# Optimization experiments

Hardware: AMD Instinct MI355X
Metric: run time of the kernel (lower is better)

## Reference

```python
import jax, jax.numpy as jnp
import numpy as np

N_QUBITS = 8

def _ry(theta):
    # PennyLane RY = exp(-i theta Y/2) = [[c,-s],[s,c]]
    c = jnp.cos(theta / 2).astype(jnp.complex64)
    s = jnp.sin(theta / 2).astype(jnp.complex64)
    return jnp.stack([jnp.stack([c, -s], -1), jnp.stack([s, c], -1)], -2)

def _rz(theta):
    # PennyLane RZ = diag(e^{-i theta/2}, e^{i theta/2})
    ph = jnp.exp(-0.5j * theta.astype(jnp.complex64))
    z = jnp.zeros_like(ph)
    return jnp.stack([jnp.stack([ph, z], -1), jnp.stack([z, jnp.conj(ph)], -1)], -2)

def _apply_1q(state, U, wire):
    # state: (B, 2,...,2); U: (2,2) or (B,2,2)
    state = jnp.moveaxis(state, wire + 1, -1)
    if U.ndim == 3:
        state = jnp.einsum('bij,b...j->b...i', U, state)
    else:
        state = jnp.einsum('ij,b...j->b...i', U, state)
    return jnp.moveaxis(state, -1, wire + 1)

def _apply_cnot(state, c, t):
    state = jnp.moveaxis(state, (c + 1, t + 1), (-2, -1))
    state = jnp.concatenate([state[..., 0:1, :], state[..., 1:2, ::-1]], axis=-2)
    return jnp.moveaxis(state, (-2, -1), (c + 1, t + 1))

def _circuit(angles, qw):
    # angles: (B, 2*n_qubits), qw: (3, n_qubits, 3)
    B = angles.shape[0]
    state = jnp.zeros((B,) + (2,) * N_QUBITS, jnp.complex64)
    state = state.at[(slice(None),) + (0,) * N_QUBITS].set(1.0)
    for i in range(N_QUBITS):
        state = _apply_1q(state, _ry(angles[:, i]), i)
        state = _apply_1q(state, _rz(angles[:, i + N_QUBITS]), i)
    for layer in range(3):
        for i in range(N_QUBITS):
            phi, theta, omega = qw[layer, i]
            U = _rz(omega) @ _ry(theta) @ _rz(phi)  # Rot(phi,theta,omega)
            state = _apply_1q(state, U, i)
        for i in range(N_QUBITS - 1):
            state = _apply_cnot(state, i, i + 1)
        state = _apply_cnot(state, N_QUBITS - 1, 0)
    probs = jnp.abs(state) ** 2  # (B, 2,...,2) real
    expz = []
    for i in range(N_QUBITS):
        p = probs.sum(axis=tuple(a for a in range(1, N_QUBITS + 1) if a != i + 1))
        expz.append(p[:, 0] - p[:, 1])  # <Z_i> = p(0) - p(1)
    return jnp.stack(expz, -1)


def setup_inputs() -> dict:
    key = jax.random.key(0)
    ks = jax.random.split(key, 10)
    B = 16384
    return {
        'x': jax.random.normal(ks[0], (B, 80), jnp.float32),
        'W1': jax.random.normal(ks[1], (64, 80), jnp.float32) * 0.1,
        'b1': jax.random.normal(ks[2], (64,), jnp.float32) * 0.1,
        'W2': jax.random.normal(ks[3], (32, 64), jnp.float32) * 0.1,
        'b2': jax.random.normal(ks[4], (32,), jnp.float32) * 0.1,
        'W3': jax.random.normal(ks[5], (16, 32), jnp.float32) * 0.1,
        'b3': jax.random.normal(ks[6], (16,), jnp.float32) * 0.1,
        'qw': jax.random.normal(ks[7], (3, 8, 3), jnp.float32),
        'Wp': jax.random.normal(ks[8], (128, 8), jnp.float32) * 0.1,
        'bp': jax.random.normal(ks[9], (128,), jnp.float32) * 0.1,
    }


def reference(x, W1, b1, W2, b2, W3, b3, qw, Wp, bp):
    h = jnp.tanh(x @ W1.T + b1)
    h = jnp.tanh(h @ W2.T + b2)
    angles = h @ W3.T + b3          # (B, 16)
    z = _circuit(angles, qw)        # (B, 8) PauliZ expectations
    return z @ Wp.T + bp            # (B, 128)
```

## Files before the change

### kernel.cpp

```cpp
#include <hip/hip_runtime.h>

typedef float v2f __attribute__((ext_vector_type(2)));

#define WPB 4
#define NE  4

__device__ __forceinline__ float xorf(float v, int sb) {
  return __int_as_float(__float_as_int(v) ^ sb);
}

__device__ __forceinline__ void pkfma_ip(v2f a, v2f b, v2f& acc) {
  asm("v_pk_fma_f32 %0, %1, %2, %0" : "+v"(acc) : "v"(a), "v"(b));
}
__device__ __forceinline__ v2f pkmul_bl(v2f c, v2f v) {
  v2f r; asm("v_pk_mul_f32 %0, %1, %2 op_sel:[0,0] op_sel_hi:[0,1]"
             : "=v"(r) : "v"(c), "v"(v)); return r;
}
__device__ __forceinline__ void pkfma_bl(v2f c, v2f v, v2f& acc) {
  asm("v_pk_fma_f32 %0, %1, %2, %0 op_sel:[0,0,0] op_sel_hi:[0,1,1]"
      : "+v"(acc) : "v"(c), "v"(v));
}
__device__ __forceinline__ void pkfma_bl_n(v2f c, v2f v, v2f& acc) {
  asm("v_pk_fma_f32 %0, %1, %2, %0 op_sel:[0,0,0] op_sel_hi:[0,1,1] neg_lo:[1,0,0] neg_hi:[1,0,0]"
      : "+v"(acc) : "v"(c), "v"(v));
}
__device__ __forceinline__ void pkfma_bh_i(v2f c, v2f v, v2f& acc) {
  asm("v_pk_fma_f32 %0, %1, %2, %0 op_sel:[1,1,0] op_sel_hi:[1,0,1] neg_lo:[1,0,0]"
      : "+v"(acc) : "v"(c), "v"(v));
}
__device__ __forceinline__ void pkfma_bh_mi(v2f c, v2f v, v2f& acc) {
  asm("v_pk_fma_f32 %0, %1, %2, %0 op_sel:[1,1,0] op_sel_hi:[1,0,1] neg_hi:[1,0,0]"
      : "+v"(acc) : "v"(c), "v"(v));
}
__device__ __forceinline__ v2f cmul(v2f a, v2f b) {
  v2f r = pkmul_bl(a, b);
  pkfma_bh_i(a, b, r);
  return r;
}

template<int M>
__device__ __forceinline__ float xch(float v, int a32) {
  if constexpr (M == 32)
    return __int_as_float(__builtin_amdgcn_ds_bpermute(a32, __float_as_int(v)));
  else if constexpr (M == 16 || M == 4)
    return __int_as_float(__builtin_amdgcn_ds_swizzle(__float_as_int(v), (M << 10) | 0x1f));
  else if constexpr (M == 8) {
    int i = __float_as_int(v);
    return __int_as_float(__builtin_amdgcn_update_dpp(i, i, 0x128, 0xF, 0xF, false));
  } else if constexpr (M == 2) {
    int i = __float_as_int(v);
    return __int_as_float(__builtin_amdgcn_update_dpp(i, i, 0x4E, 0xF, 0xF, false));
  } else {
    int i = __float_as_int(v);
    return __int_as_float(__builtin_amdgcn_update_dpp(i, i, 0xB1, 0xF, 0xF, false));
  }
}
template<int M>
__device__ __forceinline__ v2f xch2(v2f v, int a32) {
  v2f r; r.x = xch<M>(v.x, a32); r.y = xch<M>(v.y, a32); return r;
}
__device__ __forceinline__ v2f bperm2(int addr, v2f v) {
  v2f r;
  r.x = __int_as_float(__builtin_amdgcn_ds_bpermute(addr, __float_as_int(v.x)));
  r.y = __int_as_float(__builtin_amdgcn_ds_bpermute(addr, __float_as_int(v.y)));
  return r;
}

__device__ __forceinline__ void gpair(v2f& a, v2f& b, v2f P1, v2f P2) {
  v2f na = pkmul_bl(P1, a);
  pkfma_bh_i(P1, a, na);
  pkfma_bl(P2, b, na);
  pkfma_bh_i(P2, b, na);
  v2f nb = pkmul_bl(P1, b);
  pkfma_bh_mi(P1, b, nb);
  pkfma_bl_n(P2, a, nb);
  pkfma_bh_i(P2, a, nb);
  a = na; b = nb;
}
__device__ __forceinline__ v2f glane(v2f a, v2f p, v2f P1, v2f P2) {
  v2f t = pkmul_bl(P1, a);
  pkfma_bh_i(P1, a, t);
  pkfma_bl(P2, p, t);
  pkfma_bh_i(P2, p, t);
  return t;
}

template<int W>
__device__ __forceinline__ void gate_all(v2f* S, v2f P1, v2f P2,
                                         const int* sb, int a32) {
  if constexpr (W == 0) {
    #pragma unroll
    for (int e = 0; e < NE; ++e) {
      gpair(S[4*e+0], S[4*e+2], P1, P2); gpair(S[4*e+1], S[4*e+3], P1, P2);
    }
  } else if constexpr (W == 1) {
    #pragma unroll
    for (int e = 0; e < NE; ++e) {
      gpair(S[4*e+0], S[4*e+1], P1, P2); gpair(S[4*e+2], S[4*e+3], P1, P2);
    }
  } else {
    constexpr int M = 1 << (7 - W);
    const int s = sb[W - 2];
    v2f P1s = P1; P1s.y = xorf(P1.y, s);
    v2f P2s = P2; P2s.x = xorf(P2.x, s);
    #pragma unroll
    for (int e = 0; e < NE; ++e) {
      v2f p0 = xch2<M>(S[4*e+0], a32), p1 = xch2<M>(S[4*e+1], a32),
          p2 = xch2<M>(S[4*e+2], a32), p3 = xch2<M>(S[4*e+3], a32);
      S[4*e+0] = glane(S[4*e+0], p0, P1s, P2s);
      S[4*e+1] = glane(S[4*e+1], p1, P1s, P2s);
      S[4*e+2] = glane(S[4*e+2], p2, P1s, P2s);
      S[4*e+3] = glane(S[4*e+3], p3, P1s, P2s);
    }
  }
}

__device__ __forceinline__ void build_state(v2f* S, const float4* csW, int lane) {
  v2f g[6];
  #pragma unroll
  for (int w = 2; w < 8; ++w) {
    float4 c = csW[w];
    v2f P1 = (v2f){c.x, c.y};
    v2f nc2 = (v2f){-c.z, c.w};
    bool shi = ((lane >> (7 - w)) & 1) != 0;
    g[w - 2] = shi ? nc2 : P1;
  }
  v2f c23 = cmul(g[0], g[1]);
  v2f c45 = cmul(g[2], g[3]);
  v2f c67 = cmul(g[4], g[5]);
  v2f common = cmul(c23, cmul(c45, c67));
  float4 c0 = csW[0], c1 = csW[1];
  v2f P10 = (v2f){c0.x, c0.y}, m0 = (v2f){-c0.z, c0.w};
  v2f P11 = (v2f){c1.x, c1.y}, m1 = (v2f){-c1.z, c1.w};
  S[0] = cmul(cmul(P10, P11), common);
  S[1] = cmul(cmul(P10, m1 ), common);
  S[2] = cmul(cmul(m0 , P11), common);
  S[3] = cmul(cmul(m0 , m1 ), common);
}

__device__ __forceinline__ void cnot_ring(v2f* S, int addrA, int addrB, int lane) {
  { v2f t = S[2]; S[2] = S[3]; S[3] = t; }
  S[0] = bperm2(addrA, S[0]); S[2] = bperm2(addrA, S[2]);
  S[1] = bperm2(addrB, S[1]); S[3] = bperm2(addrB, S[3]);
  bool c0 = (lane & 1) != 0;
  v2f t0 = S[0], t1 = S[1];
  S[0] = c0 ? S[2] : S[0]; S[2] = c0 ? t0 : S[2];
  S[1] = c0 ? S[3] : S[1]; S[3] = c0 ? t1 : S[3];
}

__device__ __forceinline__ void readout(const v2f* S, int lane, const int* sb,
                                        int a32, float* z) {
  float p0 = S[0].x*S[0].x + S[0].y*S[0].y;
  float p1 = S[1].x*S[1].x + S[1].y*S[1].y;
  float p2 = S[2].x*S[2].x + S[2].y*S[2].y;
  float p3 = S[3].x*S[3].x + S[3].y*S[3].y;
  float E = (p0 + p3) - (p1 + p2);
  float F = (p0 + p2) - (p1 + p3);
  float Fv = xorf(F, (__popc(lane) & 1) << 31);
  float Sm = E, d1, d2, d3, d4, d5, d6;
  { float p = xch<32>(Sm, a32); d1 = xorf(Sm - p, sb[0]); Sm += p; }
  { float p = xch<16>(Sm, a32); Sm += p;
    float q = xch<16>(d1, a32); d2 = xorf(d1 - q, sb[1]); d1 += q; }
  { float p = xch<8>(Sm, a32); Sm += p;
    float q = xch<8>(d1, a32); d1 += q;
    float r = xch<8>(d2, a32); d3 = xorf(d2 - r, sb[2]); d2 += r; }
  { float p = xch<4>(Sm, a32); Sm += p;
    float q = xch<4>(d1, a32); d1 += q;
    float r = xch<4>(d2, a32); d2 += r;
    float t = xch<4>(d3, a32); d4 = xorf(d3 - t, sb[3]); d3 += t; }
  { float p = xch<2>(Sm, a32); Sm += p;
    float q = xch<2>(d1, a32); d1 += q;
    float r = xch<2>(d2, a32); d2 += r;
    float t = xch<2>(d3, a32); d3 += t;
    float w = xch<2>(d4, a32); d5 = xorf(d4 - w, sb[4]); d4 += w; }
  { float p = xch<1>(Sm, a32); Sm += p;
    float q = xch<1>(d1, a32); d1 += q;
    float r = xch<1>(d2, a32); d2 += r;
    float t = xch<1>(d3, a32); d3 += t;
    float w = xch<1>(d4, a32); d4 += w;
    float v = xch<1>(d5, a32); d6 = xorf(d5 - v, sb[5]); d5 += v; }
  Fv += xch<32>(Fv, a32); Fv += xch<16>(Fv, a32); Fv += xch<8>(Fv, a32);
  Fv += xch<4>(Fv, a32);  Fv += xch<2>(Fv, a32);  Fv += xch<1>(Fv, a32);
  z[0] = Fv; z[1] = Sm; z[2] = d1; z[3] = d2;
  z[4] = d3; z[5] = d4; z[6] = d5; z[7] = d6;
}

__device__ __forceinline__ float fast_tanh(float x) {
  float e = __expf(2.f * x);
  return 1.f - 2.f * __builtin_amdgcn_rcpf(e + 1.f);
}
__device__ __forceinline__ v2f vlo(float4 v) { return (v2f){v.x, v.y}; }
__device__ __forceinline__ v2f vhi(float4 v) { return (v2f){v.z, v.w}; }

__global__ void prep_rot_kernel(const float* __restrict__ qw, float* __restrict__ U) {
  int t = threadIdx.x;
  if (t < 24) {
    float phi = qw[t*3+0], theta = qw[t*3+1], omega = qw[t*3+2];
    float st, ct; sincosf(0.5f*theta, &st, &ct);
    float sa, ca; sincosf(0.5f*(phi+omega), &sa, &ca);
    float sd, cd; sincosf(0.5f*(phi-omega), &sd, &cd);
    float4 o; o.x = ct*ca; o.y = -ct*sa; o.z = -st*cd; o.w = -st*sd;
    ((float4*)U)[t] = o;
  }
}

__global__ __launch_bounds__(64*WPB) void qblock_kernel(
    const float* __restrict__ x,  const float* __restrict__ W1, const float* __restrict__ b1,
    const float* __restrict__ W2, const float* __restrict__ b2,
    const float* __restrict__ W3, const float* __restrict__ b3,
    const float* __restrict__ Urot, const float* __restrict__ Wp, const float* __restrict__ bp,
    float* __restrict__ out, int B4)
{
  __shared__ float  h1s[WPB][NE][64];
  __shared__ float  h2s[WPB][NE][32];
  __shared__ v2f    cs [WPB][NE][16];
  __shared__ float4 csW[WPB][NE][8];

  const int lane = threadIdx.x & 63;
  const int wv   = threadIdx.x >> 6;
  int bw = blockIdx.x * WPB + wv;
  if (bw >= B4) bw = B4 - 1;
  bw = __builtin_amdgcn_readfirstlane(bw);
  const int e0 = NE * bw;
  const v2f* Ug2 = (const v2f*)Urot;

  {
    const float4* wr = (const float4*)(W1 + lane * 80);
    float bv = b1[lane];
    v2f a0[NE], a1[NE];
    #pragma unroll
    for (int e = 0; e < NE; ++e) { a0[e] = (v2f){bv, 0.f}; a1[e] = (v2f){0.f, 0.f}; }
    #pragma unroll
    for (int k = 0; k < 20; ++k) {
      float4 wk = wr[k];
      #pragma unroll
      for (int e = 0; e < NE; ++e) {
        float4 xk = ((const float4*)(x + (size_t)(e0 + e) * 80))[k];
        pkfma_ip(vlo(xk), vlo(wk), a0[e]);
        pkfma_ip(vhi(xk), vhi(wk), a1[e]);
      }
    }
    #pragma unroll
    for (int e = 0; e < NE; ++e)
      h1s[wv][e][lane] = fast_tanh((a0[e].x + a0[e].y) + (a1[e].x + a1[e].y));
  }
  __threadfence_block();

  {
    const int ep = lane >> 5, row = lane & 31;
    const float4* wr = (const float4*)(W2 + row * 64);
    const float4* hvA = (const float4*)(&h1s[wv][2*ep+0][0]);
    const float4* hvB = (const float4*)(&h1s[wv][2*ep+1][0]);
    v2f aA0 = (v2f){b2[row], 0.f}, aA1 = (v2f){0.f, 0.f};
    v2f aB0 = aA0, aB1 = aA1;
    #pragma unroll
    for (int k = 0; k < 16; ++k) {
      float4 wk = wr[k], hA = hvA[k], hB = hvB[k];
      pkfma_ip(vlo(hA), vlo(wk), aA0); pkfma_ip(vhi(hA), vhi(wk), aA1);
      pkfma_ip(vlo(hB), vlo(wk), aB0); pkfma_ip(vhi(hB), vhi(wk), aB1);
    }
    h2s[wv][2*ep+0][row] = fast_tanh((aA0.x + aA0.y) + (aA1.x + aA1.y));
    h2s[wv][2*ep+1][row] = fast_tanh((aB0.x + aB0.y) + (aB1.x + aB1.y));
  }
  __threadfence_block();

  {
    const int e = lane >> 4, row = lane & 15;
    const float4* hv = (const float4*)(&h2s[wv][e][0]);
    const float4* wr = (const float4*)(W3 + row * 32);
    v2f ac0 = (v2f){b3[row], 0.f}, ac1 = (v2f){0.f, 0.f};
    #pragma unroll
    for (int k = 0; k < 8; ++k) {
      float4 hk = hv[k], wk = wr[k];
      pkfma_ip(vlo(hk), vlo(wk), ac0);
      pkfma_ip(vhi(hk), vhi(wk), ac1);
    }
    float sh, ch; __sincosf(0.5f * ((ac0.x + ac0.y) + (ac1.x + ac1.y)), &sh, &ch);
    cs[wv][e][row] = (v2f){ch, sh};
  }
  __threadfence_block();

  if (lane < 32) {
    const int e = lane >> 3, k = lane & 7;
    v2f yy = cs[wv][e][k], zz = cs[wv][e][k + 8];
    v2f u1 = (v2f){  yy.x * zz.x, -yy.x * zz.y };
    v2f u2 = (v2f){ -yy.y * zz.x,  yy.y * zz.y };
    v2f cu1 = (v2f){ u1.x, -u1.y };
    v2f cu2 = (v2f){ u2.x, -u2.y };
    v2f r1 = Ug2[2 * k], r2 = Ug2[2 * k + 1];
    v2f P1c = cmul(r1, u1);
    pkfma_bl_n(r2, cu2, P1c);
    pkfma_bh_mi(r2, cu2, P1c);
    v2f P2c = cmul(r1, u2);
    pkfma_bl(r2, cu1, P2c);
    pkfma_bh_i(r2, cu1, P2c);
    csW[wv][e][k] = make_float4(P1c.x, P1c.y, P2c.x, P2c.y);
  }
  __threadfence_block();

  const int a32 = (lane ^ 32) << 2;
  const int sb[6] = { (lane&32)<<26, (lane&16)<<27, (lane&8)<<28,
                      (lane&4)<<29, (lane&2)<<30, (lane&1)<<31 };
  const int addrA = ((lane ^ (lane >> 1)) & 63) << 2;
  const int addrB = addrA ^ 128;

  v2f S[4 * NE];
  #pragma unroll
  for (int e = 0; e < NE; ++e) build_state(&S[4*e], &csW[wv][e][0], lane);
  #pragma unroll
  for (int e = 0; e < NE; ++e) cnot_ring(&S[4*e], addrA, addrB, lane);

  #define LGB(l, i) { v2f P1 = Ug2[((l)*8+(i))*2], P2 = Ug2[((l)*8+(i))*2+1]; \
    gate_all<i>(S, P1, P2, sb, a32); }
  LGB(1,0) LGB(1,1) LGB(1,2) LGB(1,3) LGB(1,4) LGB(1,5) LGB(1,6) LGB(1,7)
  #pragma unroll
  for (int e = 0; e < NE; ++e) cnot_ring(&S[4*e], addrA, addrB, lane);
  LGB(2,0) LGB(2,1) LGB(2,2) LGB(2,3) LGB(2,4) LGB(2,5) LGB(2,6) LGB(2,7)
  #undef LGB

  const int r0 = 2 * lane;
  const float4* wp = (const float4*)(Wp + r0 * 8);
  float4 w0v = wp[0], w1v = wp[1], w2v = wp[2], w3v = wp[3];
  float2 bpv = ((const float2*)bp)[lane];
  #pragma unroll
  for (int e = 0; e < NE; ++e) {
    float z[8];
    readout(&S[4*e], lane, sb, a32, z);
    float o0 = bpv.x + z[0]*w0v.x + z[1]*w0v.y + z[2]*w0v.z + z[3]*w0v.w
                     + z[4]*w1v.x + z[5]*w1v.y + z[6]*w1v.z + z[7]*w1v.w;
    float o1 = bpv.y + z[0]*w2v.x + z[1]*w2v.y + z[2]*w2v.z + z[3]*w2v.w
                     + z[4]*w3v.x + z[5]*w3v.y + z[6]*w3v.z + z[7]*w3v.w;
    ((float2*)(out + (size_t)(e0 + e) * 128))[lane] = make_float2(o0, o1);
  }
}

extern "C" void kernel_launch(void* const* d_in, const int* in_sizes, int n_in,
                              void* d_out, int out_size, void* d_ws, size_t ws_size,
                              hipStream_t stream) {
  const float* x  = (const float*)d_in[0];
  const float* W1 = (const float*)d_in[1];
  const float* b1 = (const float*)d_in[2];
  const float* W2 = (const float*)d_in[3];
  const float* b2 = (const float*)d_in[4];
  const float* W3 = (const float*)d_in[5];
  const float* b3 = (const float*)d_in[6];
  const float* qw = (const float*)d_in[7];
  const float* Wp = (const float*)d_in[8];
  const float* bp = (const float*)d_in[9];
  float* out = (float*)d_out;
  float* Urot = (float*)d_ws;

  const int B = in_sizes[0] / 80;
  const int B4 = B / NE;
  prep_rot_kernel<<<1, 64, 0, stream>>>(qw, Urot);
  const int grid = (B4 + WPB - 1) / WPB;
  qblock_kernel<<<grid, 64 * WPB, 0, stream>>>(x, W1, b1, W2, b2, W3, b3,
                                               Urot, Wp, bp, out, B4);
}
```

Baseline: 42.20 us.

## Process eight batch elements per wave and pair readout reductions

Doubles the number of batch elements each wavefront simulates from four to eight. The MLP stages are reshaped to cover the extra elements, and the readout reduces two states at once so each cross-lane exchange carries packed pairs. The aim is to amortise weight loads, fixed per-wave costs and shuffle latency over more elements. In exchange it raises register pressure from a doubled state array, which may lower occupancy, and halves the grid size.

New measurement: 41.87 us. About the same (-0.8%).

```diff
diff --git a/kernel.cpp b/kernel.cpp
--- a/kernel.cpp
+++ b/kernel.cpp
@@ -3,10 +3,13 @@
 typedef float v2f __attribute__((ext_vector_type(2)));
 
 #define WPB 4
-#define NE  4
+#define NE  8
 
 __device__ __forceinline__ float xorf(float v, int sb) {
   return __int_as_float(__float_as_int(v) ^ sb);
+}
+__device__ __forceinline__ v2f xor2(v2f v, int sb) {
+  return (v2f){xorf(v.x, sb), xorf(v.y, sb)};
 }
 
 __device__ __forceinline__ void pkfma_ip(v2f a, v2f b, v2f& acc) {
@@ -148,39 +151,39 @@
   S[1] = c0 ? S[3] : S[1]; S[3] = c0 ? t1 : S[3];
 }
 
-__device__ __forceinline__ void readout(const v2f* S, int lane, const int* sb,
-                                        int a32, float* z) {
-  float p0 = S[0].x*S[0].x + S[0].y*S[0].y;
-  float p1 = S[1].x*S[1].x + S[1].y*S[1].y;
-  float p2 = S[2].x*S[2].x + S[2].y*S[2].y;
-  float p3 = S[3].x*S[3].x + S[3].y*S[3].y;
-  float E = (p0 + p3) - (p1 + p2);
-  float F = (p0 + p2) - (p1 + p3);
-  float Fv = xorf(F, (__popc(lane) & 1) << 31);
-  float Sm = E, d1, d2, d3, d4, d5, d6;
-  { float p = xch<32>(Sm, a32); d1 = xorf(Sm - p, sb[0]); Sm += p; }
-  { float p = xch<16>(Sm, a32); Sm += p;
-    float q = xch<16>(d1, a32); d2 = xorf(d1 - q, sb[1]); d1 += q; }
-  { float p = xch<8>(Sm, a32); Sm += p;
-    float q = xch<8>(d1, a32); d1 += q;
-    float r = xch<8>(d2, a32); d3 = xorf(d2 - r, sb[2]); d2 += r; }
-  { float p = xch<4>(Sm, a32); Sm += p;
-    float q = xch<4>(d1, a32); d1 += q;
-    float r = xch<4>(d2, a32); d2 += r;
-    float t = xch<4>(d3, a32); d4 = xorf(d3 - t, sb[3]); d3 += t; }
-  { float p = xch<2>(Sm, a32); Sm += p;
-    float q = xch<2>(d1, a32); d1 += q;
-    float r = xch<2>(d2, a32); d2 += r;
-    float t = xch<2>(d3, a32); d3 += t;
-    float w = xch<2>(d4, a32); d5 = xorf(d4 - w, sb[4]); d4 += w; }
-  { float p = xch<1>(Sm, a32); Sm += p;
-    float q = xch<1>(d1, a32); d1 += q;
-    float r = xch<1>(d2, a32); d2 += r;
-    float t = xch<1>(d3, a32); d3 += t;
-    float w = xch<1>(d4, a32); d4 += w;
-    float v = xch<1>(d5, a32); d6 = xorf(d5 - v, sb[5]); d5 += v; }
-  Fv += xch<32>(Fv, a32); Fv += xch<16>(Fv, a32); Fv += xch<8>(Fv, a32);
-  Fv += xch<4>(Fv, a32);  Fv += xch<2>(Fv, a32);  Fv += xch<1>(Fv, a32);
+__device__ __forceinline__ void readout2(const v2f* SA, const v2f* SB,
+                                         int lane, const int* sb, int a32, v2f* z) {
+  v2f p0 = (v2f){fmaf(SA[0].x,SA[0].x,SA[0].y*SA[0].y), fmaf(SB[0].x,SB[0].x,SB[0].y*SB[0].y)};
+  v2f p1 = (v2f){fmaf(SA[1].x,SA[1].x,SA[1].y*SA[1].y), fmaf(SB[1].x,SB[1].x,SB[1].y*SB[1].y)};
+  v2f p2 = (v2f){fmaf(SA[2].x,SA[2].x,SA[2].y*SA[2].y), fmaf(SB[2].x,SB[2].x,SB[2].y*SB[2].y)};
+  v2f p3 = (v2f){fmaf(SA[3].x,SA[3].x,SA[3].y*SA[3].y), fmaf(SB[3].x,SB[3].x,SB[3].y*SB[3].y)};
+  v2f E = (p0 + p3) - (p1 + p2);
+  v2f F = (p0 + p2) - (p1 + p3);
+  v2f Fv = xor2(F, (__popc(lane) & 1) << 31);
+  v2f Sm = E, d1, d2, d3, d4, d5, d6;
+  { v2f p = xch2<32>(Sm, a32); d1 = xor2(Sm - p, sb[0]); Sm += p; }
+  { v2f p = xch2<16>(Sm, a32); Sm += p;
+    v2f q = xch2<16>(d1, a32); d2 = xor2(d1 - q, sb[1]); d1 += q; }
+  { v2f p = xch2<8>(Sm, a32); Sm += p;
+    v2f q = xch2<8>(d1, a32); d1 += q;
+    v2f r = xch2<8>(d2, a32); d3 = xor2(d2 - r, sb[2]); d2 += r; }
+  { v2f p = xch2<4>(Sm, a32); Sm += p;
+    v2f q = xch2<4>(d1, a32); d1 += q;
+    v2f r = xch2<4>(d2, a32); d2 += r;
+    v2f t = xch2<4>(d3, a32); d4 = xor2(d3 - t, sb[3]); d3 += t; }
+  { v2f p = xch2<2>(Sm, a32); Sm += p;
+    v2f q = xch2<2>(d1, a32); d1 += q;
+    v2f r = xch2<2>(d2, a32); d2 += r;
+    v2f t = xch2<2>(d3, a32); d3 += t;
+    v2f w = xch2<2>(d4, a32); d5 = xor2(d4 - w, sb[4]); d4 += w; }
+  { v2f p = xch2<1>(Sm, a32); Sm += p;
+    v2f q = xch2<1>(d1, a32); d1 += q;
+    v2f r = xch2<1>(d2, a32); d2 += r;
+    v2f t = xch2<1>(d3, a32); d3 += t;
+    v2f w = xch2<1>(d4, a32); d4 += w;
+    v2f v = xch2<1>(d5, a32); d6 = xor2(d5 - v, sb[5]); d5 += v; }
+  Fv += xch2<32>(Fv, a32); Fv += xch2<16>(Fv, a32); Fv += xch2<8>(Fv, a32);
+  Fv += xch2<4>(Fv, a32);  Fv += xch2<2>(Fv, a32);  Fv += xch2<1>(Fv, a32);
   z[0] = Fv; z[1] = Sm; z[2] = d1; z[3] = d2;
   z[4] = d3; z[5] = d4; z[6] = d5; z[7] = d6;
 }
@@ -209,7 +212,7 @@
     const float* __restrict__ W2, const float* __restrict__ b2,
     const float* __restrict__ W3, const float* __restrict__ b3,
     const float* __restrict__ Urot, const float* __restrict__ Wp, const float* __restrict__ bp,
-    float* __restrict__ out, int B4)
+    float* __restrict__ out, int B8)
 {
   __shared__ float  h1s[WPB][NE][64];
   __shared__ float  h2s[WPB][NE][32];
@@ -219,7 +222,7 @@
   const int lane = threadIdx.x & 63;
   const int wv   = threadIdx.x >> 6;
   int bw = blockIdx.x * WPB + wv;
-  if (bw >= B4) bw = B4 - 1;
+  if (bw >= B8) bw = B8 - 1;
   bw = __builtin_amdgcn_readfirstlane(bw);
   const int e0 = NE * bw;
   const v2f* Ug2 = (const v2f*)Urot;
@@ -247,40 +250,53 @@
   __threadfence_block();
 
   {
-    const int ep = lane >> 5, row = lane & 31;
+    const int eg = (lane >> 5) * 4, row = lane & 31;
     const float4* wr = (const float4*)(W2 + row * 64);
-    const float4* hvA = (const float4*)(&h1s[wv][2*ep+0][0]);
-    const float4* hvB = (const float4*)(&h1s[wv][2*ep+1][0]);
-    v2f aA0 = (v2f){b2[row], 0.f}, aA1 = (v2f){0.f, 0.f};
-    v2f aB0 = aA0, aB1 = aA1;
+    v2f a0[4], a1[4];
+    #pragma unroll
+    for (int j = 0; j < 4; ++j) { a0[j] = (v2f){b2[row], 0.f}; a1[j] = (v2f){0.f, 0.f}; }
     #pragma unroll
     for (int k = 0; k < 16; ++k) {
-      float4 wk = wr[k], hA = hvA[k], hB = hvB[k];
-      pkfma_ip(vlo(hA), vlo(wk), aA0); pkfma_ip(vhi(hA), vhi(wk), aA1);
-      pkfma_ip(vlo(hB), vlo(wk), aB0); pkfma_ip(vhi(hB), vhi(wk), aB1);
-    }
-    h2s[wv][2*ep+0][row] = fast_tanh((aA0.x + aA0.y) + (aA1.x + aA1.y));
-    h2s[wv][2*ep+1][row] = fast_tanh((aB0.x + aB0.y) + (aB1.x + aB1.y));
+      float4 wk = wr[k];
+      #pragma unroll
+      for (int j = 0; j < 4; ++j) {
+        float4 hk = ((const float4*)(&h1s[wv][eg + j][0]))[k];
+        pkfma_ip(vlo(hk), vlo(wk), a0[j]);
+        pkfma_ip(vhi(hk), vhi(wk), a1[j]);
+      }
+    }
+    #pragma unroll
+    for (int j = 0; j < 4; ++j)
+      h2s[wv][eg + j][row] = fast_tanh((a0[j].x + a0[j].y) + (a1[j].x + a1[j].y));
   }
   __threadfence_block();
 
   {
-    const int e = lane >> 4, row = lane & 15;
-    const float4* hv = (const float4*)(&h2s[wv][e][0]);
+    const int eb = lane >> 4, row = lane & 15;
     const float4* wr = (const float4*)(W3 + row * 32);
-    v2f ac0 = (v2f){b3[row], 0.f}, ac1 = (v2f){0.f, 0.f};
+    v2f a0[2], a1[2];
+    #pragma unroll
+    for (int j = 0; j < 2; ++j) { a0[j] = (v2f){b3[row], 0.f}; a1[j] = (v2f){0.f, 0.f}; }
     #pragma unroll
     for (int k = 0; k < 8; ++k) {
-      float4 hk = hv[k], wk = wr[k];
-      pkfma_ip(vlo(hk), vlo(wk), ac0);
-      pkfma_ip(vhi(hk), vhi(wk), ac1);
-    }
-    float sh, ch; __sincosf(0.5f * ((ac0.x + ac0.y) + (ac1.x + ac1.y)), &sh, &ch);
-    cs[wv][e][row] = (v2f){ch, sh};
+      float4 wk = wr[k];
+      #pragma unroll
+      for (int j = 0; j < 2; ++j) {
+        float4 hk = ((const float4*)(&h2s[wv][eb + 4*j][0]))[k];
+        pkfma_ip(vlo(hk), vlo(wk), a0[j]);
+        pkfma_ip(vhi(hk), vhi(wk), a1[j]);
+      }
+    }
+    #pragma unroll
+    for (int j = 0; j < 2; ++j) {
+      float sh, ch;
+      __sincosf(0.5f * ((a0[j].x + a0[j].y) + (a1[j].x + a1[j].y)), &sh, &ch);
+      cs[wv][eb + 4*j][row] = (v2f){ch, sh};
+    }
   }
   __threadfence_block();
 
-  if (lane < 32) {
+  {
     const int e = lane >> 3, k = lane & 7;
     v2f yy = cs[wv][e][k], zz = cs[wv][e][k + 8];
     v2f u1 = (v2f){  yy.x * zz.x, -yy.x * zz.y };
@@ -323,14 +339,17 @@
   float4 w0v = wp[0], w1v = wp[1], w2v = wp[2], w3v = wp[3];
   float2 bpv = ((const float2*)bp)[lane];
   #pragma unroll
-  for (int e = 0; e < NE; ++e) {
-    float z[8];
-    readout(&S[4*e], lane, sb, a32, z);
-    float o0 = bpv.x + z[0]*w0v.x + z[1]*w0v.y + z[2]*w0v.z + z[3]*w0v.w
-                     + z[4]*w1v.x + z[5]*w1v.y + z[6]*w1v.z + z[7]*w1v.w;
-    float o1 = bpv.y + z[0]*w2v.x + z[1]*w2v.y + z[2]*w2v.z + z[3]*w2v.w
-                     + z[4]*w3v.x + z[5]*w3v.y + z[6]*w3v.z + z[7]*w3v.w;
-    ((float2*)(out + (size_t)(e0 + e) * 128))[lane] = make_float2(o0, o1);
+  for (int ep = 0; ep < NE / 2; ++ep) {
+    v2f z[8];
+    readout2(&S[8*ep], &S[8*ep + 4], lane, sb, a32, z);
+    v2f o0 = (v2f){bpv.x, bpv.x};
+    v2f o1 = (v2f){bpv.y, bpv.y};
+    o0 += z[0]*w0v.x + z[1]*w0v.y + z[2]*w0v.z + z[3]*w0v.w
+        + z[4]*w1v.x + z[5]*w1v.y + z[6]*w1v.z + z[7]*w1v.w;
+    o1 += z[0]*w2v.x + z[1]*w2v.y + z[2]*w2v.z + z[3]*w2v.w
+        + z[4]*w3v.x + z[5]*w3v.y + z[6]*w3v.z + z[7]*w3v.w;
+    ((float2*)(out + (size_t)(e0 + 2*ep    ) * 128))[lane] = make_float2(o0.x, o1.x);
+    ((float2*)(out + (size_t)(e0 + 2*ep + 1) * 128))[lane] = make_float2(o0.y, o1.y);
   }
 }
 
@@ -351,9 +370,9 @@
   float* Urot = (float*)d_ws;
 
   const int B = in_sizes[0] / 80;
-  const int B4 = B / NE;
+  const int B8 = B / NE;
   prep_rot_kernel<<<1, 64, 0, stream>>>(qw, Urot);
-  const int grid = (B4 + WPB - 1) / WPB;
+  const int grid = (B8 + WPB - 1) / WPB;
   qblock_kernel<<<grid, 64 * WPB, 0, stream>>>(x, W1, b1, W2, b2, W3, b3,
-                                               Urot, Wp, bp, out, B4);
-}
+                                               Urot, Wp, bp, out, B8);
+}
```
